# Kernel optimization log

Hardware: AMD Instinct MI355X
Metric: run time of the kernel (lower is better)

## Reference

```python
import jax, jax.numpy as jnp
import numpy as np

QMAX = 127.0  # 8-bit narrow-range symmetric: values in [-127, 127]


def _quantize_per_tensor(t):
    """Symmetric per-tensor int8 quantization (narrow range, like Brevitas Int8*PerTensorFloat).
    Returns (int8 codes as int32 for matmul, float scale)."""
    scale = jnp.max(jnp.abs(t)) / QMAX
    q = jnp.clip(jnp.round(t / scale), -QMAX, QMAX).astype(jnp.int8)
    return q, scale


def setup_inputs() -> dict:
    key = jax.random.key(0)
    k_x, k_w, k_b = jax.random.split(key, 3)
    size_in, size_out, n = 1024, 1024, 32768
    x = jax.random.normal(k_x, (n, size_in), dtype=jnp.float32)
    # kaiming_uniform_(a=sqrt(5)) on [size_out, size_in] -> bound = 1/sqrt(size_in)
    bound = 1.0 / np.sqrt(size_in)
    weight = jax.random.uniform(k_w, (size_out, size_in), dtype=jnp.float32,
                                minval=-bound, maxval=bound)
    bias = jax.random.uniform(k_b, (size_out,), dtype=jnp.float32,
                              minval=-bound, maxval=bound)
    return {"x": x, "weight": weight, "bias": bias}


def reference(x, weight, bias):
    # Quantize activations and weights to int8 per-tensor symmetric.
    qx, sx = _quantize_per_tensor(x)        # [N, K] int8, scalar scale
    qw, sw = _quantize_per_tensor(weight)   # [M, K] int8, scalar scale
    # Approximate-multiplier GEMM modeled as exact int8 MAC with int32 accum
    # (mul8s_acc is the accurate 8-bit multiplier LUT).
    acc = jnp.matmul(qx.astype(jnp.int32), qw.astype(jnp.int32).T)  # [N, M] int32
    # Rescale: output / ((QMAX/input_scale) * (QMAX/weight_scale)) with
    # Brevitas scale conventions == acc * sx * sw here.
    out = acc.astype(jnp.float32) * (sx * sw)
    return out + bias
```

## Files before the change

### kernel.cpp

```cpp
#include <hip/hip_runtime.h>
#include <cstdint>
#include <cstddef>


typedef int v4i __attribute__((ext_vector_type(4)));

#define QMAXF 127.0f
#define KDIM 1024
#define MDIM 1024
#define NBX 512
#define NBW 32

__global__ __launch_bounds__(256) void absmax_partial(
    const float4* __restrict__ x, int nx4,
    const float4* __restrict__ w, int nw4,
    float* __restrict__ partials) {
  const int b = blockIdx.x;
  const bool isw = (b >= NBX);
  const float4* __restrict__ p = isw ? w : x;
  const int n4 = isw ? nw4 : nx4;
  const int nb = isw ? NBW : NBX;
  const int bb = isw ? (b - NBX) : b;
  const int stride = nb * 256;

  float m0 = 0.f, m1 = 0.f, m2 = 0.f, m3 = 0.f;
  int i = bb * 256 + threadIdx.x;
  for (; i + 3 * stride < n4; i += 4 * stride) {
    float4 v0 = p[i], v1 = p[i + stride], v2 = p[i + 2 * stride],
           v3 = p[i + 3 * stride];
    m0 = fmaxf(m0, fmaxf(fmaxf(fabsf(v0.x), fabsf(v0.y)),
                         fmaxf(fabsf(v0.z), fabsf(v0.w))));
    m1 = fmaxf(m1, fmaxf(fmaxf(fabsf(v1.x), fabsf(v1.y)),
                         fmaxf(fabsf(v1.z), fabsf(v1.w))));
    m2 = fmaxf(m2, fmaxf(fmaxf(fabsf(v2.x), fabsf(v2.y)),
                         fmaxf(fabsf(v2.z), fabsf(v2.w))));
    m3 = fmaxf(m3, fmaxf(fmaxf(fabsf(v3.x), fabsf(v3.y)),
                         fmaxf(fabsf(v3.z), fabsf(v3.w))));
  }
  for (; i < n4; i += stride) {
    float4 v = p[i];
    m0 = fmaxf(m0, fmaxf(fmaxf(fabsf(v.x), fabsf(v.y)),
                         fmaxf(fabsf(v.z), fabsf(v.w))));
  }
  float m = fmaxf(fmaxf(m0, m1), fmaxf(m2, m3));
  for (int off = 32; off; off >>= 1) m = fmaxf(m, __shfl_down(m, off, 64));
  __shared__ float wm[4];
  const int lane = threadIdx.x & 63, wid = threadIdx.x >> 6;
  if (lane == 0) wm[wid] = m;
  __syncthreads();
  if (threadIdx.x == 0)
    partials[b] = fmaxf(fmaxf(wm[0], wm[1]), fmaxf(wm[2], wm[3]));
}

__global__ __launch_bounds__(256) void quant2(
    const float4* __restrict__ x, int nx16,
    const float4* __restrict__ w, int nw16,
    const float* __restrict__ partials,
    v4i* __restrict__ qx, v4i* __restrict__ qw,
    float* __restrict__ amax_out) {
  const int sel = blockIdx.y;
  const float* pp = partials + (sel ? NBX : 0);
  const int np = sel ? NBW : NBX;
  float m = 0.f;
  for (int i = threadIdx.x; i < np; i += 256) m = fmaxf(m, pp[i]);
  for (int off = 32; off; off >>= 1) m = fmaxf(m, __shfl_down(m, off, 64));
  __shared__ float wm[4];
  __shared__ float bmax;
  const int lane = threadIdx.x & 63, wid = threadIdx.x >> 6;
  if (lane == 0) wm[wid] = m;
  __syncthreads();
  if (threadIdx.x == 0) {
    float bm = fmaxf(fmaxf(wm[0], wm[1]), fmaxf(wm[2], wm[3]));
    bmax = bm;
    if (blockIdx.x == 0) amax_out[sel] = bm;
  }
  __syncthreads();
  const float amax = bmax;
  const float r = QMAXF / amax;

  const float4* __restrict__ p = sel ? w : x;
  const int n16 = sel ? nw16 : nx16;
  v4i* __restrict__ q = sel ? qw : qx;

  for (int i = blockIdx.x * 256 + threadIdx.x; i < n16;
       i += gridDim.x * 256) {
    float4 v0 = p[4 * i], v1 = p[4 * i + 1], v2 = p[4 * i + 2],
           v3 = p[4 * i + 3];
    v4i o;
#define QPK(V)                                                         \
  ((((int)fminf(fmaxf(rintf((V).x * r), -QMAXF), QMAXF)) & 255) |      \
   ((((int)fminf(fmaxf(rintf((V).y * r), -QMAXF), QMAXF)) & 255) << 8) | \
   ((((int)fminf(fmaxf(rintf((V).z * r), -QMAXF), QMAXF)) & 255) << 16) | \
   ((((int)fminf(fmaxf(rintf((V).w * r), -QMAXF), QMAXF)) & 255) << 24))
    o[0] = QPK(v0);
    o[1] = QPK(v1);
    o[2] = QPK(v2);
    o[3] = QPK(v3);
#undef QPK
    q[i] = o;
  }
}

__device__ __forceinline__ void ld_lds16(const void* g, void* l) {
  __builtin_amdgcn_global_load_lds(
      (__attribute__((address_space(1))) void*)(void*)g,
      (__attribute__((address_space(3))) void*)l, 16, 0, 0);
}

__global__ __launch_bounds__(256) void gemm_i8(
    const char* __restrict__ qx, const char* __restrict__ qw,
    const float* __restrict__ bias, const float* __restrict__ amax,
    float* __restrict__ out) {
  __shared__ __align__(16) char smA[128 * 128];
  __shared__ __align__(16) char smB[128 * 128];

  const int tid = threadIdx.x;
  const int wave = tid >> 6;
  const int lane = tid & 63;
  const int bm = blockIdx.x;
  const int bn = blockIdx.y;
  const int wn = wave >> 1;
  const int wm = wave & 1;

  const char* xb = qx + (size_t)(bn * 128) * KDIM;
  const char* wb = qw + (size_t)(bm * 128) * KDIM;

  v4i acc[4][4] = {};

  const int lrow = lane >> 3;
  const int sgx = (lane & 7) ^ lrow;

  for (int kt = 0; kt < 8; ++kt) {
    const int kb = kt * 128;
#pragma unroll
    for (int c = 0; c < 4; ++c) {
      const int rbase = c * 32 + wave * 8;
      ld_lds16(xb + (size_t)(rbase + lrow) * KDIM + kb + sgx * 16,
               smA + rbase * 128);
      ld_lds16(wb + (size_t)(rbase + lrow) * KDIM + kb + sgx * 16,
               smB + rbase * 128);
    }
    __syncthreads();

#pragma unroll
    for (int kc = 0; kc < 2; ++kc) {
      const int s = kc * 4 + (lane >> 4);
      v4i a[4], b[4];
#pragma unroll
      for (int i = 0; i < 4; ++i) {
        const int r = wn * 64 + i * 16 + (lane & 15);
        a[i] = *(const v4i*)(smA + r * 128 + ((s ^ (r & 7)) * 16));
      }
#pragma unroll
      for (int j = 0; j < 4; ++j) {
        const int r = wm * 64 + j * 16 + (lane & 15);
        b[j] = *(const v4i*)(smB + r * 128 + ((s ^ (r & 7)) * 16));
      }
#pragma unroll
      for (int i = 0; i < 4; ++i)
#pragma unroll
        for (int j = 0; j < 4; ++j)
          acc[i][j] = __builtin_amdgcn_mfma_i32_16x16x64_i8(a[i], b[j],
                                                            acc[i][j], 0, 0, 0);
    }
    __syncthreads();
  }

  const float s = (amax[0] / QMAXF) * (amax[1] / QMAXF);
  const int mcol = bm * 128 + wm * 64 + (lane & 15);
  const int nbase = bn * 128 + wn * 64 + ((lane >> 4) << 2);
  float bv[4];
#pragma unroll
  for (int j = 0; j < 4; ++j) bv[j] = bias[mcol + j * 16];
#pragma unroll
  for (int i = 0; i < 4; ++i) {
#pragma unroll
    for (int r = 0; r < 4; ++r) {
      const int n = nbase + i * 16 + r;
      float* orow = out + (size_t)n * MDIM + mcol;
#pragma unroll
      for (int j = 0; j < 4; ++j)
        orow[j * 16] = (float)acc[i][j][r] * s + bv[j];
    }
  }
}

extern "C" void kernel_launch(void* const* d_in, const int* in_sizes, int n_in,
                              void* d_out, int out_size, void* d_ws, size_t ws_size,
                              hipStream_t stream) {
  const float* x = (const float*)d_in[0];
  const float* w = (const float*)d_in[1];
  const float* bias = (const float*)d_in[2];
  float* out = (float*)d_out;

  const int NX = in_sizes[0];
  const int NW = in_sizes[1];
  const int N = NX / KDIM;

  float* amax = (float*)d_ws;
  float* partials = (float*)((char*)d_ws + 64);
  char* qx = (char*)d_ws + 4096;
  char* qw = qx + (size_t)NX;

  absmax_partial<<<NBX + NBW, 256, 0, stream>>>(
      (const float4*)x, NX / 4, (const float4*)w, NW / 4, partials);

  dim3 qgrid(1024, 2);
  quant2<<<qgrid, 256, 0, stream>>>((const float4*)x, NX / 16,
                                    (const float4*)w, NW / 16, partials,
                                    (v4i*)qx, (v4i*)qw, amax);

  dim3 ggrid(MDIM / 128, N / 128);
  gemm_i8<<<ggrid, 256, 0, stream>>>(qx, qw, bias, amax, out);
}
```

Before: 298.2 us.

## Rewrite int8 GEMM with 256x256 tiles, double-buffered LDS and phased prefetch

```diff
diff --git a/kernel.cpp b/kernel.cpp
--- a/kernel.cpp
+++ b/kernel.cpp
@@ -101,86 +101,138 @@
   }
 }
 
+
 __device__ __forceinline__ void ld_lds16(const void* g, void* l) {
   __builtin_amdgcn_global_load_lds(
       (__attribute__((address_space(1))) void*)(void*)g,
       (__attribute__((address_space(3))) void*)l, 16, 0, 0);
 }
 
-__global__ __launch_bounds__(256) void gemm_i8(
+#define SBAR() asm volatile("s_barrier" ::: "memory")
+#define WAITV(n) asm volatile("s_waitcnt vmcnt(" #n ")" ::: "memory")
+
+#define BK 128
+#define BMT 256
+#define BNT 256
+
+__global__ __launch_bounds__(512, 2) void gemm_i8(
     const char* __restrict__ qx, const char* __restrict__ qw,
     const float* __restrict__ bias, const float* __restrict__ amax,
     float* __restrict__ out) {
-  __shared__ __align__(16) char smA[128 * 128];
-  __shared__ __align__(16) char smB[128 * 128];
+  __shared__ __align__(16) char smA[2][BNT * BK];
+  __shared__ __align__(16) char smB[2][BMT * BK];
 
   const int tid = threadIdx.x;
   const int wave = tid >> 6;
   const int lane = tid & 63;
-  const int bm = blockIdx.x;
-  const int bn = blockIdx.y;
+
+  const int p = blockIdx.x;
+  const int lb = (p & 7) * 64 + (p >> 3);
+  const int bm = lb >> 7;
+  const int bn = lb & 127;
+
   const int wn = wave >> 1;
   const int wm = wave & 1;
 
-  const char* xb = qx + (size_t)(bn * 128) * KDIM;
-  const char* wb = qw + (size_t)(bm * 128) * KDIM;
-
-  v4i acc[4][4] = {};
+  const char* __restrict__ xb = qx + (size_t)bn * BNT * KDIM;
+  const char* __restrict__ wb = qw + (size_t)bm * BMT * KDIM;
 
   const int lrow = lane >> 3;
   const int sgx = (lane & 7) ^ lrow;
-
-  for (int kt = 0; kt < 8; ++kt) {
-    const int kb = kt * 128;
-#pragma unroll
-    for (int c = 0; c < 4; ++c) {
-      const int rbase = c * 32 + wave * 8;
-      ld_lds16(xb + (size_t)(rbase + lrow) * KDIM + kb + sgx * 16,
-               smA + rbase * 128);
-      ld_lds16(wb + (size_t)(rbase + lrow) * KDIM + kb + sgx * 16,
-               smB + rbase * 128);
-    }
-    __syncthreads();
-
-#pragma unroll
-    for (int kc = 0; kc < 2; ++kc) {
-      const int s = kc * 4 + (lane >> 4);
-      v4i a[4], b[4];
-#pragma unroll
-      for (int i = 0; i < 4; ++i) {
-        const int r = wn * 64 + i * 16 + (lane & 15);
-        a[i] = *(const v4i*)(smA + r * 128 + ((s ^ (r & 7)) * 16));
-      }
-#pragma unroll
-      for (int j = 0; j < 4; ++j) {
-        const int r = wm * 64 + j * 16 + (lane & 15);
-        b[j] = *(const v4i*)(smB + r * 128 + ((s ^ (r & 7)) * 16));
-      }
-#pragma unroll
-      for (int i = 0; i < 4; ++i)
-#pragma unroll
-        for (int j = 0; j < 4; ++j)
-          acc[i][j] = __builtin_amdgcn_mfma_i32_16x16x64_i8(a[i], b[j],
-                                                            acc[i][j], 0, 0, 0);
-    }
-    __syncthreads();
-  }
-
-  const float s = (amax[0] / QMAXF) * (amax[1] / QMAXF);
-  const int mcol = bm * 128 + wm * 64 + (lane & 15);
-  const int nbase = bn * 128 + wn * 64 + ((lane >> 4) << 2);
-  float bv[4];
-#pragma unroll
-  for (int j = 0; j < 4; ++j) bv[j] = bias[mcol + j * 16];
+  const int gcol = sgx * 16;
+
+  v4i acc[4][8] = {};
+
+#define STAGE_A(bufc, kb, half) do {                                        \
+    _Pragma("unroll") for (int c = 0; c < 2; ++c) {                         \
+      const int sg = wave * 2 + c;                                          \
+      const int rb = (sg >> 2) * 64 + (half) * 32 + (sg & 3) * 8;           \
+      ld_lds16(xb + (size_t)(rb + lrow) * KDIM + (kb) + gcol,               \
+               &smA[bufc][rb * BK]);                                        \
+    }                                                                       \
+  } while (0)
+#define STAGE_B(bufc, kb, half) do {                                        \
+    _Pragma("unroll") for (int c = 0; c < 2; ++c) {                         \
+      const int sg = wave * 2 + c;                                          \
+      const int rb = (sg >> 3) * 128 + (half) * 64 + (sg & 7) * 8;          \
+      ld_lds16(wb + (size_t)(rb + lrow) * KDIM + (kb) + gcol,               \
+               &smB[bufc][rb * BK]);                                        \
+    }                                                                       \
+  } while (0)
+
+#define PHASE(bufc, ih, jh, STG, WT) do {                                   \
+    v4i a_[2][2], b_[2][4];                                                 \
+    _Pragma("unroll") for (int ks = 0; ks < 2; ++ks) {                      \
+      const int sw = ((ks * 4 + (lane >> 4)) * 16) ^ ((lane & 7) * 16);     \
+      _Pragma("unroll") for (int i = 0; i < 2; ++i) {                       \
+        const int r = wn * 64 + (ih) * 32 + i * 16 + (lane & 15);           \
+        a_[ks][i] = *(const v4i*)(&smA[bufc][r * BK + sw]);                 \
+      }                                                                     \
+      _Pragma("unroll") for (int j = 0; j < 4; ++j) {                       \
+        const int r = wm * 128 + (jh) * 64 + j * 16 + (lane & 15);          \
+        b_[ks][j] = *(const v4i*)(&smB[bufc][r * BK + sw]);                 \
+      }                                                                     \
+    }                                                                       \
+    STG;                                                                    \
+    SBAR();                                                                 \
+    __builtin_amdgcn_s_setprio(1);                                          \
+    _Pragma("unroll") for (int ks = 0; ks < 2; ++ks)                        \
+      _Pragma("unroll") for (int i = 0; i < 2; ++i)                         \
+        _Pragma("unroll") for (int j = 0; j < 4; ++j)                       \
+          acc[(ih) * 2 + i][(jh) * 4 + j] =                                 \
+              __builtin_amdgcn_mfma_i32_16x16x64_i8(                        \
+                  a_[ks][i], b_[ks][j], acc[(ih) * 2 + i][(jh) * 4 + j],    \
+                  0, 0, 0);                                                 \
+    __builtin_amdgcn_s_setprio(0);                                          \
+    WT;                                                                     \
+    SBAR();                                                                 \
+  } while (0)
+
+#define GROUP(bufc, kb1)                                                    \
+    PHASE(bufc, 0, 0, STAGE_A((bufc) ^ 1, kb1, 0), WAITV(4));               \
+    PHASE(bufc, 0, 1, STAGE_B((bufc) ^ 1, kb1, 0), WAITV(4));               \
+    PHASE(bufc, 1, 0, STAGE_B((bufc) ^ 1, kb1, 1), (void)0);                \
+    PHASE(bufc, 1, 1, STAGE_A((bufc) ^ 1, kb1, 1), WAITV(4));
+
+  STAGE_A(0, 0, 0);
+  STAGE_B(0, 0, 0);
+  STAGE_B(0, 0, 1);
+  STAGE_A(0, 0, 1);
+  WAITV(4);
+  SBAR();
+
+  GROUP(0, 1 * BK);
+  GROUP(1, 2 * BK);
+  GROUP(0, 3 * BK);
+  GROUP(1, 4 * BK);
+  GROUP(0, 5 * BK);
+  GROUP(1, 6 * BK);
+  GROUP(0, 7 * BK);
+  PHASE(1, 0, 0, (void)0, WAITV(2));
+  PHASE(1, 0, 1, (void)0, WAITV(0));
+  PHASE(1, 1, 0, (void)0, (void)0);
+  PHASE(1, 1, 1, (void)0, (void)0);
+
+#undef GROUP
+#undef PHASE
+#undef STAGE_A
+#undef STAGE_B
+
+  const float sfac = (amax[0] / QMAXF) * (amax[1] / QMAXF);
+  const int mcol = bm * BMT + wm * 128 + (lane & 15);
+  const int nb0 = bn * BNT + wn * 64 + ((lane >> 4) << 2);
+  float bv[8];
+#pragma unroll
+  for (int j = 0; j < 8; ++j) bv[j] = bias[mcol + j * 16];
 #pragma unroll
   for (int i = 0; i < 4; ++i) {
 #pragma unroll
     for (int r = 0; r < 4; ++r) {
-      const int n = nbase + i * 16 + r;
+      const int n = nb0 + i * 16 + r;
       float* orow = out + (size_t)n * MDIM + mcol;
 #pragma unroll
-      for (int j = 0; j < 4; ++j)
-        orow[j * 16] = (float)acc[i][j][r] * s + bv[j];
+      for (int j = 0; j < 8; ++j)
+        orow[j * 16] = (float)acc[i][j][r] * sfac + bv[j];
     }
   }
 }
@@ -210,6 +262,5 @@
                                     (const float4*)w, NW / 16, partials,
                                     (v4i*)qx, (v4i*)qw, amax);
 
-  dim3 ggrid(MDIM / 128, N / 128);
-  gemm_i8<<<ggrid, 256, 0, stream>>>(qx, qw, bias, amax, out);
-}
+  gemm_i8<<<dim3(512), 512, 0, stream>>>(qx, qw, bias, amax, out);
+}
```

Result: no change. 297.6 us (-0.2%).
